# Kernel tuning notes

Measured on AMD Instinct MI355X. Metric: run time of the kernel, lower is better.

Reference implementation:

```python
import jax, jax.numpy as jnp
import numpy as np

N = 50000      # nodes
DEG = 16       # fixed out-degree per row
E = N * DEG    # edges (CSR nnz)
H = 128        # hidden_size
NH = 8         # num_heads


def setup_inputs() -> dict:
    key = jax.random.key(0)
    ks = jax.random.split(key, 8)
    s = 1.0 / np.sqrt(H)
    h = jax.random.normal(ks[0], (N, H), jnp.float32)
    Wq = jax.random.normal(ks[1], (H, H), jnp.float32) * s
    bq = jax.random.normal(ks[2], (H,), jnp.float32) * 0.02
    Wk = jax.random.normal(ks[3], (H, H), jnp.float32) * s
    bk = jax.random.normal(ks[4], (H,), jnp.float32) * 0.02
    Wv = jax.random.normal(ks[5], (H, H), jnp.float32) * s
    bv = jax.random.normal(ks[6], (H,), jnp.float32) * 0.02
    row_ptr = jnp.arange(N + 1, dtype=jnp.int32) * DEG            # fixed-degree CSR
    col_ind = jax.random.randint(ks[7], (E,), 0, N, dtype=jnp.int32)
    return {"h": h, "Wq": Wq, "bq": bq, "Wk": Wk, "bk": bk, "Wv": Wv, "bv": bv,
            "row_ptr": row_ptr, "col_ind": col_ind, "num_heads": NH}


def reference(h, Wq, bq, Wk, bk, Wv, bv, row_ptr, col_ind, num_heads):
    n = h.shape[0]
    hidden = h.shape[1]
    head_dim = hidden // num_heads
    scaling = head_dim ** (-0.5)
    e = col_ind.shape[0]
    # CSR nnz -> row index per edge
    row = (jnp.searchsorted(row_ptr, jnp.arange(e, dtype=row_ptr.dtype), side="right") - 1).astype(jnp.int32)

    # projections; reshape to (N, head_dim, num_heads) exactly as in the torch code
    q = ((h @ Wq.T + bq) * scaling).reshape(n, head_dim, num_heads)
    k = (h @ Wk.T + bk).reshape(n, head_dim, num_heads)
    v = (h @ Wv.T + bv).reshape(n, head_dim, num_heads)

    # bsddmm: per-edge, per-head dot product over head_dim
    scores = jnp.einsum("edh,edh->eh", q[row], k[col_ind])      # [E, NH]

    # sparse row-wise softmax (segment softmax over edges of each row)
    m = jax.ops.segment_max(scores, row, num_segments=n)        # [N, NH]
    ex = jnp.exp(scores - m[row])
    denom = jax.ops.segment_sum(ex, row, num_segments=n)        # [N, NH]
    attn = ex / denom[row]                                      # [E, NH]

    # bspmm: out[i] = sum_{j in nbr(i)} attn[ij] * v[j]
    out = jax.ops.segment_sum(attn[:, None, :] * v[col_ind], row, num_segments=n)  # [N, head_dim, NH]
    return out.reshape(n, -1)
```

## Files before the change

kernel.cpp:

```cpp
#include <hip/hip_runtime.h>
#include <hip/hip_bf16.h>


typedef unsigned short ushort_t;
typedef unsigned int uint32;
typedef short short8 __attribute__((ext_vector_type(8)));
typedef short short4v __attribute__((ext_vector_type(4)));
typedef float f32x4 __attribute__((ext_vector_type(4)));
typedef float f32x2 __attribute__((ext_vector_type(2)));

#define HID 128
#define DEG 16
#define OSTRIDE_LDS 132

__device__ __forceinline__ float bf2f(ushort_t u) {
  uint32 x = ((uint32)u) << 16;
  return __builtin_bit_cast(float, x);
}
__device__ __forceinline__ ushort_t f2bf(float f) {
  uint32 u = __builtin_bit_cast(uint32, f);
  u += 0x7fffu + ((u >> 16) & 1u);
  return (ushort_t)(u >> 16);
}

__device__ __forceinline__ void split2(float x, float y, uint32& hi, uint32& lo) {
  __hip_bfloat162 h2 = __float22bfloat162_rn(float2{x, y});
  __builtin_memcpy(&hi, &h2, 4);
  float hx = __builtin_bit_cast(float, hi << 16);
  float hy = __builtin_bit_cast(float, hi & 0xffff0000u);
  __hip_bfloat162 l2 = __float22bfloat162_rn(float2{x - hx, y - hy});
  __builtin_memcpy(&lo, &l2, 4);
}

__device__ __forceinline__ void split8v(float4 a, float4 b, short8& hi, short8& lo) {
  uint32* hu = (uint32*)&hi;
  uint32* lu = (uint32*)&lo;
  split2(a.x, a.y, hu[0], lu[0]);
  split2(a.z, a.w, hu[1], lu[1]);
  split2(b.x, b.y, hu[2], lu[2]);
  split2(b.z, b.w, hu[3], lu[3]);
}

__device__ __forceinline__ void split8p(const float* __restrict__ p, short8& hi, short8& lo) {
  float4 a = *(const float4*)p;
  float4 b = *(const float4*)(p + 4);
  split8v(a, b, hi, lo);
}

__global__ __launch_bounds__(256) void prep_kernel(
    const float* __restrict__ Wq, const float* __restrict__ Wk,
    const float* __restrict__ Wv,
    ushort_t* __restrict__ whi, ushort_t* __restrict__ wlo) {
  const int idx8 = (blockIdx.x * 256 + threadIdx.x) * 8;
  const float* W = (idx8 < 16384) ? Wq : (idx8 < 32768) ? Wk : Wv;
  const int off = idx8 & 16383;
  short8 hi, lo;
  split8p(W + off, hi, lo);
  *(short8*)(whi + idx8) = hi;
  *(short8*)(wlo + idx8) = lo;
}

__global__ __launch_bounds__(256) void qkv_fused_kernel(
    const float* __restrict__ h,
    const float* __restrict__ bq, const float* __restrict__ bk,
    const float* __restrict__ bv,
    const ushort_t* __restrict__ whi, const ushort_t* __restrict__ wlo,
    ushort_t* __restrict__ qs, ushort_t* __restrict__ kvt,
    int n) {
  __shared__ __align__(16) char lds_b[32 * 1024];
  __shared__ ushort_t lds_r[4][32 * OSTRIDE_LDS];

  const int wave = threadIdx.x >> 6;
  const int l = threadIdx.x & 63;
  const int lm = l & 15;
  const int lq = l >> 4;
  const int m0 = blockIdx.x * 128 + wave * 32;

  int ar0 = m0 + lm;        if (ar0 >= n) ar0 = n - 1;
  int ar1 = m0 + 16 + lm;   if (ar1 >= n) ar1 = n - 1;
  const float* ap0 = h + (size_t)ar0 * HID + lq * 8;
  const float* ap1 = h + (size_t)ar1 * HID + lq * 8;
  short8 ah0[4], al0[4], ah1[4], al1[4];
#pragma unroll
  for (int kt = 0; kt < 4; kt++) {
    split8p(ap0 + kt * 32, ah0[kt], al0[kt]);
    split8p(ap1 + kt * 32, ah1[kt], al1[kt]);
  }

#pragma unroll 1
  for (int p = 0; p < 3; p++) {
    const ushort_t* __restrict__ Wh = whi + p * 16384;
    const ushort_t* __restrict__ Wl = wlo + p * 16384;
    const float* __restrict__ bias = (p == 0) ? bq : (p == 1) ? bk : bv;
    ushort_t* __restrict__ outp = (p == 0) ? qs : (p == 1) ? kvt : kvt + 128;
    const float scale = (p == 0) ? 0.25f : 1.0f;

    f32x4 acc[2][8];
#pragma unroll
    for (int f = 0; f < 2; f++)
#pragma unroll
      for (int t = 0; t < 8; t++) acc[f][t] = (f32x4){0.f, 0.f, 0.f, 0.f};

#pragma unroll
    for (int jj = 0; jj < 8; jj++) {
      const int j = wave * 8 + jj, t = j >> 2, kt = j & 3;
      const ushort_t* gp = Wh + (t * 16 + lm) * HID + kt * 32 + lq * 8;
      __builtin_amdgcn_global_load_lds(
          (const __attribute__((address_space(1))) void*)gp,
          (__attribute__((address_space(3))) void*)(lds_b + j * 1024 + l * 16),
          16, 0, 0);
    }
    __syncthreads();
#pragma unroll
    for (int kt = 0; kt < 4; kt++) {
#pragma unroll
      for (int t = 0; t < 8; t++) {
        short8 bh = *(const short8*)(lds_b + (t * 4 + kt) * 1024 + l * 16);
        acc[0][t] = __builtin_amdgcn_mfma_f32_16x16x32_bf16(ah0[kt], bh, acc[0][t], 0, 0, 0);
        acc[0][t] = __builtin_amdgcn_mfma_f32_16x16x32_bf16(al0[kt], bh, acc[0][t], 0, 0, 0);
        acc[1][t] = __builtin_amdgcn_mfma_f32_16x16x32_bf16(ah1[kt], bh, acc[1][t], 0, 0, 0);
        acc[1][t] = __builtin_amdgcn_mfma_f32_16x16x32_bf16(al1[kt], bh, acc[1][t], 0, 0, 0);
      }
    }
    __syncthreads();

#pragma unroll
    for (int jj = 0; jj < 8; jj++) {
      const int j = wave * 8 + jj, t = j >> 2, kt = j & 3;
      const ushort_t* gp = Wl + (t * 16 + lm) * HID + kt * 32 + lq * 8;
      __builtin_amdgcn_global_load_lds(
          (const __attribute__((address_space(1))) void*)gp,
          (__attribute__((address_space(3))) void*)(lds_b + j * 1024 + l * 16),
          16, 0, 0);
    }
    __syncthreads();
#pragma unroll
    for (int kt = 0; kt < 4; kt++) {
#pragma unroll
      for (int t = 0; t < 8; t++) {
        short8 bl = *(const short8*)(lds_b + (t * 4 + kt) * 1024 + l * 16);
        acc[0][t] = __builtin_amdgcn_mfma_f32_16x16x32_bf16(ah0[kt], bl, acc[0][t], 0, 0, 0);
        acc[1][t] = __builtin_amdgcn_mfma_f32_16x16x32_bf16(ah1[kt], bl, acc[1][t], 0, 0, 0);
      }
    }
    __syncthreads();

    ushort_t* lo_ = lds_r[wave];
#pragma unroll
    for (int t = 0; t < 8; t++) {
      const int col = t * 16 + lm;
      const float bv_ = bias[col];
#pragma unroll
      for (int f = 0; f < 2; f++) {
#pragma unroll
        for (int r = 0; r < 4; r++) {
          lo_[(f * 16 + lq * 4 + r) * OSTRIDE_LDS + col] = f2bf((acc[f][t][r] + bv_) * scale);
        }
      }
    }
    asm volatile("s_waitcnt lgkmcnt(0)" ::: "memory");
    __builtin_amdgcn_wave_barrier();

    const int rr = l >> 5;
    const int ch = l & 31;
#pragma unroll
    for (int it = 0; it < 16; it++) {
      const int rw = it * 2 + rr;
      const int grow = m0 + rw;
      short4v val = *(short4v*)(lo_ + rw * OSTRIDE_LDS + ch * 4);
      if (grow < n) *(short4v*)(outp + (size_t)grow * 256 + ch * 4) = val;
    }
  }
}

__global__ __launch_bounds__(256) void attn_kernel(
    const int* __restrict__ col_ind,
    const ushort_t* __restrict__ qs, const ushort_t* __restrict__ kvt,
    float* __restrict__ out, int n) {
  __shared__ __align__(16) float lds_attn[4 * DEG * 8];

  const int wv = threadIdx.x >> 6;
  const int l = threadIdx.x & 63;
  const int lm = l & 15;
  const int lq = l >> 4;

  int row = blockIdx.x * 4 + wv;
  if (row >= n) row = n - 1;
  const int eb = row * DEG;

  const int cm = __builtin_nontemporal_load(col_ind + eb + lm);
  const ushort_t* kp = kvt + (size_t)cm * 256 + lq * 8;
  const ushort_t* qp = qs + (size_t)row * 256;

  short8 af[4];
  ushort_t qv[4];
#pragma unroll
  for (int kt = 0; kt < 4; kt++) {
    af[kt] = *(const short8*)(kp + kt * 32);
    qv[kt] = (lm < 8) ? __builtin_nontemporal_load(qp + kt * 32 + lq * 8 + lm)
                      : (ushort_t)0;
  }

  uint32 vreg[DEG];
#pragma unroll
  for (int e = 0; e < DEG; e++) {
    const int c = col_ind[eb + e];
    vreg[e] = *(const uint32*)(kvt + (size_t)c * 256 + 128 + 2 * l);
  }

  f32x4 acc = (f32x4){0.f, 0.f, 0.f, 0.f};
#pragma unroll
  for (int kt = 0; kt < 4; kt++) {
    short8 bf;
#pragma unroll
    for (int j = 0; j < 8; j++) bf[j] = (lm == j) ? (short)qv[kt] : (short)0;
    acc = __builtin_amdgcn_mfma_f32_16x16x32_bf16(af[kt], bf, acc, 0, 0, 0);
  }

  float m = fmaxf(fmaxf(acc[0], acc[1]), fmaxf(acc[2], acc[3]));
  m = fmaxf(m, __shfl_xor(m, 16, 64));
  m = fmaxf(m, __shfl_xor(m, 32, 64));
  float e0 = __expf(acc[0] - m), e1 = __expf(acc[1] - m);
  float e2 = __expf(acc[2] - m), e3 = __expf(acc[3] - m);
  float s = e0 + e1 + e2 + e3;
  s += __shfl_xor(s, 16, 64);
  s += __shfl_xor(s, 32, 64);
  const float inv = 1.0f / s;

  float* ap = &lds_attn[wv * (DEG * 8)];
  if (lm < 8) {
    ap[(lq * 4 + 0) * 8 + lm] = e0 * inv;
    ap[(lq * 4 + 1) * 8 + lm] = e1 * inv;
    ap[(lq * 4 + 2) * 8 + lm] = e2 * inv;
    ap[(lq * 4 + 3) * 8 + lm] = e3 * inv;
  }
  asm volatile("s_waitcnt lgkmcnt(0)" ::: "memory");
  __builtin_amdgcn_wave_barrier();

  const int h0 = 2 * (l & 3);
  float o0 = 0.f, o1 = 0.f;
#pragma unroll
  for (int e = 0; e < DEG; e++) {
    const float2 at = *(const float2*)(ap + e * 8 + h0);
    o0 += at.x * bf2f((ushort_t)(vreg[e] & 0xffffu));
    o1 += at.y * bf2f((ushort_t)(vreg[e] >> 16));
  }

  f32x2 o;
  o[0] = o0; o[1] = o1;
  __builtin_nontemporal_store(o, (f32x2*)(out + (size_t)row * HID + 2 * l));
}

extern "C" void kernel_launch(void* const* d_in, const int* in_sizes, int n_in,
                              void* d_out, int out_size, void* d_ws, size_t ws_size,
                              hipStream_t stream) {
  const float* h  = (const float*)d_in[0];
  const float* Wq = (const float*)d_in[1];
  const float* bq = (const float*)d_in[2];
  const float* Wk = (const float*)d_in[3];
  const float* bk = (const float*)d_in[4];
  const float* Wv = (const float*)d_in[5];
  const float* bv = (const float*)d_in[6];
  const int* col_ind = (const int*)d_in[8];

  const int n = in_sizes[0] / HID;

  ushort_t* kvt = (ushort_t*)d_ws;
  ushort_t* whi = kvt + (size_t)n * 256;
  ushort_t* wlo = whi + 3 * 16384;
  ushort_t* qs  = (ushort_t*)d_out;
  float* outf   = (float*)d_out;

  prep_kernel<<<24, 256, 0, stream>>>(Wq, Wk, Wv, whi, wlo);
  qkv_fused_kernel<<<(n + 127) / 128, 256, 0, stream>>>(h, bq, bk, bv, whi, wlo, qs, kvt, n);
  attn_kernel<<<(n + 3) / 4, 256, 0, stream>>>(col_ind, qs, kvt, outf, n);
}
```

Before: 172.7 us.

## Restructure QKV projection kernel to single-wave blocks without block barriers

The QKV projection kernel now runs one wave per block covering 32 rows, instead of four waves cooperatively loading the weight tiles. Each wave stages the full 32 KB hi/lo weight tile into LDS by itself. Block-wide __syncthreads are replaced with s_waitcnt vmcnt/lgkmcnt fences, and the output staging buffer is moved into the tail of the weight LDS buffer. This removes cross-wave barriers, but each wave now loads four times as much weight data, and 32 KB of LDS per wave may reduce occupancy.

```diff
diff --git a/kernel.cpp b/kernel.cpp
--- a/kernel.cpp
+++ b/kernel.cpp
@@ -60,7 +60,10 @@
   *(short8*)(wlo + idx8) = lo;
 }
 
-__global__ __launch_bounds__(256) void qkv_fused_kernel(
+#define FENCE_LGKM() asm volatile("s_waitcnt lgkmcnt(0)" ::: "memory")
+#define WAITV0() asm volatile("s_waitcnt vmcnt(0)" ::: "memory")
+
+__global__ __launch_bounds__(64) void qkv_fused_kernel(
     const float* __restrict__ h,
     const float* __restrict__ bq, const float* __restrict__ bk,
     const float* __restrict__ bv,
@@ -68,13 +71,12 @@
     ushort_t* __restrict__ qs, ushort_t* __restrict__ kvt,
     int n) {
   __shared__ __align__(16) char lds_b[32 * 1024];
-  __shared__ ushort_t lds_r[4][32 * OSTRIDE_LDS];
-
-  const int wave = threadIdx.x >> 6;
+  ushort_t* lds_rp = (ushort_t*)(lds_b + 24320);
+
   const int l = threadIdx.x & 63;
   const int lm = l & 15;
   const int lq = l >> 4;
-  const int m0 = blockIdx.x * 128 + wave * 32;
+  const int m0 = blockIdx.x * 32;
 
   int ar0 = m0 + lm;        if (ar0 >= n) ar0 = n - 1;
   int ar1 = m0 + 16 + lm;   if (ar1 >= n) ar1 = n - 1;
@@ -102,15 +104,15 @@
       for (int t = 0; t < 8; t++) acc[f][t] = (f32x4){0.f, 0.f, 0.f, 0.f};
 
 #pragma unroll
-    for (int jj = 0; jj < 8; jj++) {
-      const int j = wave * 8 + jj, t = j >> 2, kt = j & 3;
+    for (int j = 0; j < 32; j++) {
+      const int t = j >> 2, kt = j & 3;
       const ushort_t* gp = Wh + (t * 16 + lm) * HID + kt * 32 + lq * 8;
       __builtin_amdgcn_global_load_lds(
           (const __attribute__((address_space(1))) void*)gp,
           (__attribute__((address_space(3))) void*)(lds_b + j * 1024 + l * 16),
           16, 0, 0);
     }
-    __syncthreads();
+    WAITV0();
 #pragma unroll
     for (int kt = 0; kt < 4; kt++) {
 #pragma unroll
@@ -122,18 +124,18 @@
         acc[1][t] = __builtin_amdgcn_mfma_f32_16x16x32_bf16(al1[kt], bh, acc[1][t], 0, 0, 0);
       }
     }
-    __syncthreads();
-
-#pragma unroll
-    for (int jj = 0; jj < 8; jj++) {
-      const int j = wave * 8 + jj, t = j >> 2, kt = j & 3;
+    FENCE_LGKM();
+
+#pragma unroll
+    for (int j = 0; j < 32; j++) {
+      const int t = j >> 2, kt = j & 3;
       const ushort_t* gp = Wl + (t * 16 + lm) * HID + kt * 32 + lq * 8;
       __builtin_amdgcn_global_load_lds(
           (const __attribute__((address_space(1))) void*)gp,
           (__attribute__((address_space(3))) void*)(lds_b + j * 1024 + l * 16),
           16, 0, 0);
     }
-    __syncthreads();
+    WAITV0();
 #pragma unroll
     for (int kt = 0; kt < 4; kt++) {
 #pragma unroll
@@ -143,9 +145,8 @@
         acc[1][t] = __builtin_amdgcn_mfma_f32_16x16x32_bf16(ah1[kt], bl, acc[1][t], 0, 0, 0);
       }
     }
-    __syncthreads();
-
-    ushort_t* lo_ = lds_r[wave];
+    FENCE_LGKM();
+
 #pragma unroll
     for (int t = 0; t < 8; t++) {
       const int col = t * 16 + lm;
@@ -154,12 +155,11 @@
       for (int f = 0; f < 2; f++) {
 #pragma unroll
         for (int r = 0; r < 4; r++) {
-          lo_[(f * 16 + lq * 4 + r) * OSTRIDE_LDS + col] = f2bf((acc[f][t][r] + bv_) * scale);
+          lds_rp[(f * 16 + lq * 4 + r) * OSTRIDE_LDS + col] = f2bf((acc[f][t][r] + bv_) * scale);
         }
       }
     }
-    asm volatile("s_waitcnt lgkmcnt(0)" ::: "memory");
-    __builtin_amdgcn_wave_barrier();
+    FENCE_LGKM();
 
     const int rr = l >> 5;
     const int ch = l & 31;
@@ -167,9 +167,10 @@
     for (int it = 0; it < 16; it++) {
       const int rw = it * 2 + rr;
       const int grow = m0 + rw;
-      short4v val = *(short4v*)(lo_ + rw * OSTRIDE_LDS + ch * 4);
+      short4v val = *(short4v*)(lds_rp + rw * OSTRIDE_LDS + ch * 4);
       if (grow < n) *(short4v*)(outp + (size_t)grow * 256 + ch * 4) = val;
     }
+    FENCE_LGKM();
   }
 }
 
@@ -272,6 +273,6 @@
   float* outf   = (float*)d_out;
 
   prep_kernel<<<24, 256, 0, stream>>>(Wq, Wk, Wv, whi, wlo);
-  qkv_fused_kernel<<<(n + 127) / 128, 256, 0, stream>>>(h, bq, bk, bv, whi, wlo, qs, kvt, n);
+  qkv_fused_kernel<<<(n + 31) / 32, 64, 0, stream>>>(h, bq, bk, bv, whi, wlo, qs, kvt, n);
   attn_kernel<<<(n + 3) / 4, 256, 0, stream>>>(col_ind, qs, kvt, outf, n);
 }
```

After: 203.5 us. +17.8%, slower.

## Fuse weight bf16 hi/lo split into QKV kernel and drop prep launch

Applied to the files above, without the earlier changes.

Removes the separate prep kernel that split the fp32 weights into bf16 hi/lo halves. Each QKV block now loads the fp32 weights itself, splits them in registers, and writes both halves into a doubled 64KB LDS buffer in one phase. This cuts one kernel launch and a barrier round between the hi and lo passes, and the output staging now reuses the same LDS. In exchange every block redoes the split and reads fp32 weights, and the larger LDS footprint may lower occupancy.

```diff
diff --git a/kernel.cpp b/kernel.cpp
--- a/kernel.cpp
+++ b/kernel.cpp
@@ -47,29 +47,14 @@
   split8v(a, b, hi, lo);
 }
 
-__global__ __launch_bounds__(256) void prep_kernel(
-    const float* __restrict__ Wq, const float* __restrict__ Wk,
-    const float* __restrict__ Wv,
-    ushort_t* __restrict__ whi, ushort_t* __restrict__ wlo) {
-  const int idx8 = (blockIdx.x * 256 + threadIdx.x) * 8;
-  const float* W = (idx8 < 16384) ? Wq : (idx8 < 32768) ? Wk : Wv;
-  const int off = idx8 & 16383;
-  short8 hi, lo;
-  split8p(W + off, hi, lo);
-  *(short8*)(whi + idx8) = hi;
-  *(short8*)(wlo + idx8) = lo;
-}
-
 __global__ __launch_bounds__(256) void qkv_fused_kernel(
     const float* __restrict__ h,
-    const float* __restrict__ bq, const float* __restrict__ bk,
-    const float* __restrict__ bv,
-    const ushort_t* __restrict__ whi, const ushort_t* __restrict__ wlo,
+    const float* __restrict__ Wq, const float* __restrict__ bq,
+    const float* __restrict__ Wk, const float* __restrict__ bk,
+    const float* __restrict__ Wv, const float* __restrict__ bv,
     ushort_t* __restrict__ qs, ushort_t* __restrict__ kvt,
     int n) {
-  __shared__ __align__(16) char lds_b[32 * 1024];
-  __shared__ ushort_t lds_r[4][32 * OSTRIDE_LDS];
-
+  __shared__ __align__(16) char lds_b[64 * 1024];
   const int wave = threadIdx.x >> 6;
   const int l = threadIdx.x & 63;
   const int lm = l & 15;
@@ -89,28 +74,28 @@
 
 #pragma unroll 1
   for (int p = 0; p < 3; p++) {
-    const ushort_t* __restrict__ Wh = whi + p * 16384;
-    const ushort_t* __restrict__ Wl = wlo + p * 16384;
+    const float* __restrict__ W = (p == 0) ? Wq : (p == 1) ? Wk : Wv;
     const float* __restrict__ bias = (p == 0) ? bq : (p == 1) ? bk : bv;
     ushort_t* __restrict__ outp = (p == 0) ? qs : (p == 1) ? kvt : kvt + 128;
     const float scale = (p == 0) ? 0.25f : 1.0f;
 
-    f32x4 acc[2][8];
-#pragma unroll
-    for (int f = 0; f < 2; f++)
-#pragma unroll
-      for (int t = 0; t < 8; t++) acc[f][t] = (f32x4){0.f, 0.f, 0.f, 0.f};
-
 #pragma unroll
     for (int jj = 0; jj < 8; jj++) {
       const int j = wave * 8 + jj, t = j >> 2, kt = j & 3;
-      const ushort_t* gp = Wh + (t * 16 + lm) * HID + kt * 32 + lq * 8;
-      __builtin_amdgcn_global_load_lds(
-          (const __attribute__((address_space(1))) void*)gp,
-          (__attribute__((address_space(3))) void*)(lds_b + j * 1024 + l * 16),
-          16, 0, 0);
+      const float* wp = W + (size_t)(t * 16 + lm) * HID + kt * 32 + lq * 8;
+      short8 bh, bl;
+      split8p(wp, bh, bl);
+      *(short8*)(lds_b + j * 1024 + l * 16) = bh;
+      *(short8*)(lds_b + 32768 + j * 1024 + l * 16) = bl;
     }
     __syncthreads();
+
+    f32x4 acc[2][8];
+#pragma unroll
+    for (int f = 0; f < 2; f++)
+#pragma unroll
+      for (int t = 0; t < 8; t++) acc[f][t] = (f32x4){0.f, 0.f, 0.f, 0.f};
+
 #pragma unroll
     for (int kt = 0; kt < 4; kt++) {
 #pragma unroll
@@ -122,30 +107,18 @@
         acc[1][t] = __builtin_amdgcn_mfma_f32_16x16x32_bf16(al1[kt], bh, acc[1][t], 0, 0, 0);
       }
     }
-    __syncthreads();
-
-#pragma unroll
-    for (int jj = 0; jj < 8; jj++) {
-      const int j = wave * 8 + jj, t = j >> 2, kt = j & 3;
-      const ushort_t* gp = Wl + (t * 16 + lm) * HID + kt * 32 + lq * 8;
-      __builtin_amdgcn_global_load_lds(
-          (const __attribute__((address_space(1))) void*)gp,
-          (__attribute__((address_space(3))) void*)(lds_b + j * 1024 + l * 16),
-          16, 0, 0);
-    }
-    __syncthreads();
 #pragma unroll
     for (int kt = 0; kt < 4; kt++) {
 #pragma unroll
       for (int t = 0; t < 8; t++) {
-        short8 bl = *(const short8*)(lds_b + (t * 4 + kt) * 1024 + l * 16);
+        short8 bl = *(const short8*)(lds_b + 32768 + (t * 4 + kt) * 1024 + l * 16);
         acc[0][t] = __builtin_amdgcn_mfma_f32_16x16x32_bf16(ah0[kt], bl, acc[0][t], 0, 0, 0);
         acc[1][t] = __builtin_amdgcn_mfma_f32_16x16x32_bf16(ah1[kt], bl, acc[1][t], 0, 0, 0);
       }
     }
     __syncthreads();
 
-    ushort_t* lo_ = lds_r[wave];
+    ushort_t* lo_ = (ushort_t*)lds_b + wave * 32 * OSTRIDE_LDS;
 #pragma unroll
     for (int t = 0; t < 8; t++) {
       const int col = t * 16 + lm;
@@ -170,6 +143,7 @@
       short4v val = *(short4v*)(lo_ + rw * OSTRIDE_LDS + ch * 4);
       if (grow < n) *(short4v*)(outp + (size_t)grow * 256 + ch * 4) = val;
     }
+    __syncthreads();
   }
 }
 
@@ -266,12 +240,10 @@
   const int n = in_sizes[0] / HID;
 
   ushort_t* kvt = (ushort_t*)d_ws;
-  ushort_t* whi = kvt + (size_t)n * 256;
-  ushort_t* wlo = whi + 3 * 16384;
   ushort_t* qs  = (ushort_t*)d_out;
   float* outf   = (float*)d_out;
 
-  prep_kernel<<<24, 256, 0, stream>>>(Wq, Wk, Wv, whi, wlo);
-  qkv_fused_kernel<<<(n + 127) / 128, 256, 0, stream>>>(h, bq, bk, bv, whi, wlo, qs, kvt, n);
+  qkv_fused_kernel<<<(n + 127) / 128, 256, 0, stream>>>(
+      h, Wq, bq, Wk, bk, Wv, bv, qs, kvt, n);
   attn_kernel<<<(n + 3) / 4, 256, 0, stream>>>(col_ind, qs, kvt, outf, n);
 }
```

After: 172.3 us (median of 2 runs). Within noise of the previous version (-0.3%).
